# Performance work log

Measured on AMD Instinct MI355X. Metric: run time of the kernel, lower is better.

The kernel has to match this reference:

```python
import jax, jax.numpy as jnp
import numpy as np
from jax import lax

B, T, F, K = 128, 1024, 128, 32


def setup_inputs() -> dict:
    key = jax.random.key(0)
    k1, k2, k3 = jax.random.split(key, 3)
    inp = jax.random.normal(k1, (B, T, F), dtype=jnp.float32)
    mask = jnp.ones((B, T), dtype=bool)
    W_emit = jax.random.normal(k2, (F, K), dtype=jnp.float32) * 0.02
    transition = jax.random.normal(k3, (K, K), dtype=jnp.float32) * 0.1
    return {"input": inp, "mask": mask, "W_emit": W_emit, "transition": transition}


def reference(input, mask, W_emit, transition):
    # emissions: [B, T, K]
    emission = jnp.einsum('btf,fk->btk', input, W_emit)
    alpha0 = emission[:, 0]                      # [B, K]
    em_seq = jnp.swapaxes(emission[:, 1:], 0, 1)  # [T-1, B, K]
    mk_seq = jnp.swapaxes(mask[:, 1:], 0, 1)      # [T-1, B]

    def step(alpha, xs):
        em_t, m_t = xs
        # alpha_t[b,j] = logsumexp_i(alpha[b,i] + transition[i,j]) + em_t[b,j]
        new = jax.scipy.special.logsumexp(alpha[:, :, None] + transition[None], axis=1) + em_t
        alpha = jnp.where(m_t[:, None], new, alpha)
        return alpha, None

    alpha, _ = lax.scan(step, alpha0, (em_seq, mk_seq))
    log_z = jax.scipy.special.logsumexp(alpha, axis=-1)  # [B]
    return jnp.sum(log_z)
```

## Files before the change

### kernel.cpp

```cpp
#include <hip/hip_runtime.h>

#define Bb 128
#define Tt 1024
#define Ff 128
#define Kk 32
#define KS 36
#define KE 36
#define LOG32 3.4657359027997265f

typedef __attribute__((ext_vector_type(8))) short bf16x8;
typedef __attribute__((ext_vector_type(4))) float f32x4;

__device__ __forceinline__ float bf2f(unsigned u) {
    return __uint_as_float(u << 16);
}
__device__ __forceinline__ unsigned short f2bf(float f) {
    unsigned u = __float_as_uint(f);
    u = (u + 0x7fffu + ((u >> 16) & 1u)) >> 16;
    return (unsigned short)u;
}
__device__ __forceinline__ unsigned bfpk(float a, float b) {
    unsigned ua = (__float_as_uint(a) + 0x8000u) >> 16;
    unsigned ub = (__float_as_uint(b) + 0x8000u) & 0xffff0000u;
    return ua | ub;
}

__global__ __launch_bounds__(64, 4) void chunk_kernel(
    const float* __restrict__ inp, const int* __restrict__ mask,
    const float* __restrict__ W, const float* __restrict__ trans,
    unsigned short* __restrict__ SQ)
{
    __shared__ __align__(16) float gl[32 * KE];
    __shared__ __align__(16) unsigned short Sl[32 * KS];
    const int lane = threadIdx.x & 63;
    const int q = lane >> 4, n = lane & 15;
    const int b = blockIdx.x >> 5, c = blockIdx.x & 31;
    const int t0 = c ? c * 32 : 1;
    const int L  = c ? 32 : 31;

    const int* mbp = mask + (long)b * Tt;
    int mybit = (lane < L) ? (mbp[t0 + lane] != 0) : 0;
    const unsigned mbits = (unsigned)__ballot(mybit);

    bf16x8 A0, A1;
    #pragma unroll
    for (int j = 0; j < 8; ++j) {
        A0[j] = (short)f2bf(__expf(trans[(q * 8 + j) * Kk + n]));
        A1[j] = (short)f2bf(__expf(trans[(q * 8 + j) * Kk + 16 + n]));
    }

    const f32x4 zz = {0.f, 0.f, 0.f, 0.f};
    f32x4 E00 = zz, E01 = zz, E10 = zz, E11 = zz;
    const float* xrow = inp + ((long)b * Tt + t0) * Ff;
    #pragma unroll
    for (int kt = 0; kt < 4; ++kt) {
        const int f0 = kt * 32 + q * 8;
        float4 al0 = *(const float4*)&xrow[ n        * Ff + f0];
        float4 al1 = *(const float4*)&xrow[ n        * Ff + f0 + 4];
        float4 ah0 = *(const float4*)&xrow[(n + 16)  * Ff + f0];
        float4 ah1 = *(const float4*)&xrow[(n + 16)  * Ff + f0 + 4];
        uint4 ua = make_uint4(bfpk(al0.x, al0.y), bfpk(al0.z, al0.w),
                              bfpk(al1.x, al1.y), bfpk(al1.z, al1.w));
        uint4 ub = make_uint4(bfpk(ah0.x, ah0.y), bfpk(ah0.z, ah0.w),
                              bfpk(ah1.x, ah1.y), bfpk(ah1.z, ah1.w));
        bf16x8 Alo = __builtin_bit_cast(bf16x8, ua);
        bf16x8 Ahi = __builtin_bit_cast(bf16x8, ub);
        float wl[8], wh[8];
        #pragma unroll
        for (int jj = 0; jj < 8; ++jj) {
            wl[jj] = W[(f0 + jj) * Kk + n];
            wh[jj] = W[(f0 + jj) * Kk + 16 + n];
        }
        uint4 uc = make_uint4(bfpk(wl[0], wl[1]), bfpk(wl[2], wl[3]),
                              bfpk(wl[4], wl[5]), bfpk(wl[6], wl[7]));
        uint4 ud = make_uint4(bfpk(wh[0], wh[1]), bfpk(wh[2], wh[3]),
                              bfpk(wh[4], wh[5]), bfpk(wh[6], wh[7]));
        bf16x8 Blo = __builtin_bit_cast(bf16x8, uc);
        bf16x8 Bhi = __builtin_bit_cast(bf16x8, ud);
        E00 = __builtin_amdgcn_mfma_f32_16x16x32_bf16(Alo, Blo, E00, 0, 0, 0);
        E01 = __builtin_amdgcn_mfma_f32_16x16x32_bf16(Alo, Bhi, E01, 0, 0, 0);
        E10 = __builtin_amdgcn_mfma_f32_16x16x32_bf16(Ahi, Blo, E10, 0, 0, 0);
        E11 = __builtin_amdgcn_mfma_f32_16x16x32_bf16(Ahi, Bhi, E11, 0, 0, 0);
    }
    #pragma unroll
    for (int r = 0; r < 4; ++r) {
        gl[( q * 4 + r)      * KE + n]      = __expf(E00[r] - LOG32);
        gl[( q * 4 + r)      * KE + 16 + n] = __expf(E01[r] - LOG32);
        gl[(16 + q * 4 + r)  * KE + n]      = __expf(E10[r] - LOG32);
        gl[(16 + q * 4 + r)  * KE + 16 + n] = __expf(E11[r] - LOG32);
    }

    for (int i = lane; i < (32 * KS) / 2; i += 64)
        ((unsigned*)Sl)[i] = 0u;
    if (lane < 32) Sl[lane * KS + lane] = 0x3f80;

    for (int s = 0; s < L; ++s) {
        if (!((mbits >> s) & 1u)) continue;
        uint2 xa = *(const uint2*)&Sl[ n       * KS + q * 8];
        uint2 xb = *(const uint2*)&Sl[ n       * KS + q * 8 + 4];
        uint2 ya = *(const uint2*)&Sl[(n + 16) * KS + q * 8];
        uint2 yb = *(const uint2*)&Sl[(n + 16) * KS + q * 8 + 4];
        uint4 u0 = make_uint4(xa.x, xa.y, xb.x, xb.y);
        uint4 u1 = make_uint4(ya.x, ya.y, yb.x, yb.y);
        bf16x8 B0 = __builtin_bit_cast(bf16x8, u0);
        bf16x8 B1 = __builtin_bit_cast(bf16x8, u1);
        f32x4 D00 = __builtin_amdgcn_mfma_f32_16x16x32_bf16(A0, B0, zz, 0, 0, 0);
        f32x4 D01 = __builtin_amdgcn_mfma_f32_16x16x32_bf16(A0, B1, zz, 0, 0, 0);
        f32x4 D10 = __builtin_amdgcn_mfma_f32_16x16x32_bf16(A1, B0, zz, 0, 0, 0);
        f32x4 D11 = __builtin_amdgcn_mfma_f32_16x16x32_bf16(A1, B1, zz, 0, 0, 0);
        float4 g0 = *(const float4*)&gl[s * KE + q * 4];
        float4 g1 = *(const float4*)&gl[s * KE + 16 + q * 4];
        *(uint2*)&Sl[ n       * KS      + q * 4] =
            make_uint2(bfpk(D00[0] * g0.x, D00[1] * g0.y), bfpk(D00[2] * g0.z, D00[3] * g0.w));
        *(uint2*)&Sl[(n + 16) * KS      + q * 4] =
            make_uint2(bfpk(D01[0] * g0.x, D01[1] * g0.y), bfpk(D01[2] * g0.z, D01[3] * g0.w));
        *(uint2*)&Sl[ n       * KS + 16 + q * 4] =
            make_uint2(bfpk(D10[0] * g1.x, D10[1] * g1.y), bfpk(D10[2] * g1.z, D10[3] * g1.w));
        *(uint2*)&Sl[(n + 16) * KS + 16 + q * 4] =
            make_uint2(bfpk(D11[0] * g1.x, D11[1] * g1.y), bfpk(D11[2] * g1.z, D11[3] * g1.w));
    }

    unsigned short* sq = SQ + (long)(b * 32 + c) * 1024;
    #pragma unroll
    for (int it = 0; it < 2; ++it) {
        int f = it * 512 + lane * 8;
        int kk = f >> 5, n0 = f & 31;
        unsigned v[4];
        #pragma unroll
        for (int e = 0; e < 4; ++e) {
            unsigned lo = Sl[(n0 + 2 * e    ) * KS + kk];
            unsigned hi = Sl[(n0 + 2 * e + 1) * KS + kk];
            v[e] = lo | (hi << 16);
        }
        *(uint4*)(sq + f) = make_uint4(v[0], v[1], v[2], v[3]);
    }
}

__global__ __launch_bounds__(64) void apply_kernel(
    const float* __restrict__ inp, const int* __restrict__ mask,
    const float* __restrict__ W, const unsigned short* __restrict__ SQ,
    float* __restrict__ out)
{
    const int b = blockIdx.x, lane = threadIdx.x & 63, k = lane & 31;
    const int* mbp = mask + (long)b * Tt;

    const unsigned short* sqb = SQ + (long)b * 32 * 1024;
    uint4 cur[4], nxt[4];
    #pragma unroll
    for (int e = 0; e < 4; ++e) cur[e] = *(const uint4*)(sqb + k * 32 + 8 * e);
    #pragma unroll
    for (int e = 0; e < 4; ++e) nxt[e] = *(const uint4*)(sqb + 1024 + k * 32 + 8 * e);

    int cnt = 0;
    #pragma unroll
    for (int it = 0; it < 16; ++it) cnt += (mbp[it * 64 + lane] != 0) ? 1 : 0;
    #pragma unroll
    for (int off = 32; off; off >>= 1) cnt += __shfl_xor(cnt, off);
    cnt -= (mbp[0] != 0) ? 1 : 0;

    const float* x0 = inp + (long)b * Tt * Ff;
    float a0 = 0.f;
    #pragma unroll 4
    for (int f = 0; f < Ff; ++f)
        a0 = fmaf(x0[f], W[f * Kk + k], a0);

    float c0 = __int_as_float(__builtin_amdgcn_readlane(__float_as_int(a0), 0));
    float p = __expf(a0 - c0);
    float csum = c0 + (float)cnt * LOG32;

    for (int c = 0; c < 32; ++c) {
        uint4 pf[4];
        if (c + 2 < 32) {
            const unsigned short* s2 = sqb + (c + 2) * 1024 + k * 32;
            #pragma unroll
            for (int e = 0; e < 4; ++e) pf[e] = *(const uint4*)(s2 + 8 * e);
        }
        const int pi = __float_as_int(p);
        float q0 = 0.f, q1 = 0.f, q2 = 0.f, q3 = 0.f;
        #define RL(j) __int_as_float(__builtin_amdgcn_readlane(pi, (j)))
        #define ACC2(word, j, acc) \
            acc = fmaf(bf2f((word) & 0xffffu), RL(j), acc); \
            acc = fmaf(bf2f((word) >> 16),     RL((j) + 1), acc);
        ACC2(cur[0].x,  0, q0) ACC2(cur[0].y,  2, q0) ACC2(cur[0].z,  4, q0) ACC2(cur[0].w,  6, q0)
        ACC2(cur[1].x,  8, q1) ACC2(cur[1].y, 10, q1) ACC2(cur[1].z, 12, q1) ACC2(cur[1].w, 14, q1)
        ACC2(cur[2].x, 16, q2) ACC2(cur[2].y, 18, q2) ACC2(cur[2].z, 20, q2) ACC2(cur[2].w, 22, q2)
        ACC2(cur[3].x, 24, q3) ACC2(cur[3].y, 26, q3) ACC2(cur[3].z, 28, q3) ACC2(cur[3].w, 30, q3)
        #undef ACC2
        #undef RL
        float qq = (q0 + q1) + (q2 + q3);
        if (c == 15) {
            float s0 = __int_as_float(__builtin_amdgcn_readlane(__float_as_int(qq), 0));
            csum += __logf(s0);
            qq *= (1.0f / s0);
        }
        p = qq;
        #pragma unroll
        for (int e = 0; e < 4; ++e) { cur[e] = nxt[e]; nxt[e] = pf[e]; }
    }

    float sum = p;
    #pragma unroll
    for (int off = 16; off > 0; off >>= 1)
        sum += __shfl_xor(sum, off);
    if (lane == 0)
        atomicAdd(out, csum + __logf(sum));
}

extern "C" void kernel_launch(void* const* d_in, const int* in_sizes, int n_in,
                              void* d_out, int out_size, void* d_ws, size_t ws_size,
                              hipStream_t stream)
{
    const float* inp   = (const float*)d_in[0];
    const int*   mask  = (const int*)d_in[1];
    const float* W     = (const float*)d_in[2];
    const float* trans = (const float*)d_in[3];
    float* out = (float*)d_out;
    unsigned short* SQ = (unsigned short*)d_ws;

    hipMemsetAsync(d_out, 0, sizeof(float), stream);
    chunk_kernel<<<dim3(Bb * 32), dim3(64), 0, stream>>>(inp, mask, W, trans, SQ);
    apply_kernel<<<dim3(Bb), dim3(64), 0, stream>>>(inp, mask, W, SQ, out);
}
```

Before: 132.0 us.

## Fuse chunk and apply kernels via last-block-done atomic counter per batch

Merges the two kernels into one. The last of the 32 chunk blocks for each batch row, found with an atomic counter and thread fences, runs the sequential apply phase. This removes a kernel launch and the grid-wide dependency gap, at the cost of an extra memset for the counters and tail blocks that run serially. It also widens the shared-memory row stride so B fragments load as single 16-byte reads, and uses the hip bf16 pair conversion intrinsic (round-to-nearest-even) instead of manual packing.

```diff
diff --git a/kernel.cpp b/kernel.cpp
--- a/kernel.cpp
+++ b/kernel.cpp
@@ -1,10 +1,11 @@
 #include <hip/hip_runtime.h>
+#include <hip/hip_bf16.h>
 
 #define Bb 128
 #define Tt 1024
 #define Ff 128
 #define Kk 32
-#define KS 36
+#define KS 40
 #define KE 36
 #define LOG32 3.4657359027997265f
 
@@ -19,16 +20,18 @@
     u = (u + 0x7fffu + ((u >> 16) & 1u)) >> 16;
     return (unsigned short)u;
 }
-__device__ __forceinline__ unsigned bfpk(float a, float b) {
-    unsigned ua = (__float_as_uint(a) + 0x8000u) >> 16;
-    unsigned ub = (__float_as_uint(b) + 0x8000u) & 0xffff0000u;
-    return ua | ub;
-}
-
-__global__ __launch_bounds__(64, 4) void chunk_kernel(
+__device__ __forceinline__ unsigned bfpk2(float a, float b) {
+    __hip_bfloat162 h = __float22bfloat162_rn(make_float2(a, b));
+    unsigned u;
+    __builtin_memcpy(&u, &h, sizeof(u));
+    return u;
+}
+
+__global__ __launch_bounds__(64, 4) void crf_kernel(
     const float* __restrict__ inp, const int* __restrict__ mask,
     const float* __restrict__ W, const float* __restrict__ trans,
-    unsigned short* __restrict__ SQ)
+    unsigned short* __restrict__ SQ, int* __restrict__ cnt,
+    float* __restrict__ out)
 {
     __shared__ __align__(16) float gl[32 * KE];
     __shared__ __align__(16) unsigned short Sl[32 * KS];
@@ -59,24 +62,26 @@
         float4 al1 = *(const float4*)&xrow[ n        * Ff + f0 + 4];
         float4 ah0 = *(const float4*)&xrow[(n + 16)  * Ff + f0];
         float4 ah1 = *(const float4*)&xrow[(n + 16)  * Ff + f0 + 4];
-        uint4 ua = make_uint4(bfpk(al0.x, al0.y), bfpk(al0.z, al0.w),
-                              bfpk(al1.x, al1.y), bfpk(al1.z, al1.w));
-        uint4 ub = make_uint4(bfpk(ah0.x, ah0.y), bfpk(ah0.z, ah0.w),
-                              bfpk(ah1.x, ah1.y), bfpk(ah1.z, ah1.w));
-        bf16x8 Alo = __builtin_bit_cast(bf16x8, ua);
-        bf16x8 Ahi = __builtin_bit_cast(bf16x8, ub);
+        uint4 ua = make_uint4(bfpk2(al0.x, al0.y), bfpk2(al0.z, al0.w),
+                              bfpk2(al1.x, al1.y), bfpk2(al1.z, al1.w));
+        uint4 ub = make_uint4(bfpk2(ah0.x, ah0.y), bfpk2(ah0.z, ah0.w),
+                              bfpk2(ah1.x, ah1.y), bfpk2(ah1.z, ah1.w));
+        bf16x8 Alo, Ahi;
+        __builtin_memcpy(&Alo, &ua, 16);
+        __builtin_memcpy(&Ahi, &ub, 16);
         float wl[8], wh[8];
         #pragma unroll
         for (int jj = 0; jj < 8; ++jj) {
             wl[jj] = W[(f0 + jj) * Kk + n];
             wh[jj] = W[(f0 + jj) * Kk + 16 + n];
         }
-        uint4 uc = make_uint4(bfpk(wl[0], wl[1]), bfpk(wl[2], wl[3]),
-                              bfpk(wl[4], wl[5]), bfpk(wl[6], wl[7]));
-        uint4 ud = make_uint4(bfpk(wh[0], wh[1]), bfpk(wh[2], wh[3]),
-                              bfpk(wh[4], wh[5]), bfpk(wh[6], wh[7]));
-        bf16x8 Blo = __builtin_bit_cast(bf16x8, uc);
-        bf16x8 Bhi = __builtin_bit_cast(bf16x8, ud);
+        uint4 uc = make_uint4(bfpk2(wl[0], wl[1]), bfpk2(wl[2], wl[3]),
+                              bfpk2(wl[4], wl[5]), bfpk2(wl[6], wl[7]));
+        uint4 ud = make_uint4(bfpk2(wh[0], wh[1]), bfpk2(wh[2], wh[3]),
+                              bfpk2(wh[4], wh[5]), bfpk2(wh[6], wh[7]));
+        bf16x8 Blo, Bhi;
+        __builtin_memcpy(&Blo, &uc, 16);
+        __builtin_memcpy(&Bhi, &ud, 16);
         E00 = __builtin_amdgcn_mfma_f32_16x16x32_bf16(Alo, Blo, E00, 0, 0, 0);
         E01 = __builtin_amdgcn_mfma_f32_16x16x32_bf16(Alo, Bhi, E01, 0, 0, 0);
         E10 = __builtin_amdgcn_mfma_f32_16x16x32_bf16(Ahi, Blo, E10, 0, 0, 0);
@@ -96,14 +101,11 @@
 
     for (int s = 0; s < L; ++s) {
         if (!((mbits >> s) & 1u)) continue;
-        uint2 xa = *(const uint2*)&Sl[ n       * KS + q * 8];
-        uint2 xb = *(const uint2*)&Sl[ n       * KS + q * 8 + 4];
-        uint2 ya = *(const uint2*)&Sl[(n + 16) * KS + q * 8];
-        uint2 yb = *(const uint2*)&Sl[(n + 16) * KS + q * 8 + 4];
-        uint4 u0 = make_uint4(xa.x, xa.y, xb.x, xb.y);
-        uint4 u1 = make_uint4(ya.x, ya.y, yb.x, yb.y);
-        bf16x8 B0 = __builtin_bit_cast(bf16x8, u0);
-        bf16x8 B1 = __builtin_bit_cast(bf16x8, u1);
+        uint4 u0 = *(const uint4*)&Sl[ n       * KS + q * 8];
+        uint4 u1 = *(const uint4*)&Sl[(n + 16) * KS + q * 8];
+        bf16x8 B0, B1;
+        __builtin_memcpy(&B0, &u0, 16);
+        __builtin_memcpy(&B1, &u1, 16);
         f32x4 D00 = __builtin_amdgcn_mfma_f32_16x16x32_bf16(A0, B0, zz, 0, 0, 0);
         f32x4 D01 = __builtin_amdgcn_mfma_f32_16x16x32_bf16(A0, B1, zz, 0, 0, 0);
         f32x4 D10 = __builtin_amdgcn_mfma_f32_16x16x32_bf16(A1, B0, zz, 0, 0, 0);
@@ -111,13 +113,13 @@
         float4 g0 = *(const float4*)&gl[s * KE + q * 4];
         float4 g1 = *(const float4*)&gl[s * KE + 16 + q * 4];
         *(uint2*)&Sl[ n       * KS      + q * 4] =
-            make_uint2(bfpk(D00[0] * g0.x, D00[1] * g0.y), bfpk(D00[2] * g0.z, D00[3] * g0.w));
+            make_uint2(bfpk2(D00[0] * g0.x, D00[1] * g0.y), bfpk2(D00[2] * g0.z, D00[3] * g0.w));
         *(uint2*)&Sl[(n + 16) * KS      + q * 4] =
-            make_uint2(bfpk(D01[0] * g0.x, D01[1] * g0.y), bfpk(D01[2] * g0.z, D01[3] * g0.w));
+            make_uint2(bfpk2(D01[0] * g0.x, D01[1] * g0.y), bfpk2(D01[2] * g0.z, D01[3] * g0.w));
         *(uint2*)&Sl[ n       * KS + 16 + q * 4] =
-            make_uint2(bfpk(D10[0] * g1.x, D10[1] * g1.y), bfpk(D10[2] * g1.z, D10[3] * g1.w));
+            make_uint2(bfpk2(D10[0] * g1.x, D10[1] * g1.y), bfpk2(D10[2] * g1.z, D10[3] * g1.w));
         *(uint2*)&Sl[(n + 16) * KS + 16 + q * 4] =
-            make_uint2(bfpk(D11[0] * g1.x, D11[1] * g1.y), bfpk(D11[2] * g1.z, D11[3] * g1.w));
+            make_uint2(bfpk2(D11[0] * g1.x, D11[1] * g1.y), bfpk2(D11[2] * g1.z, D11[3] * g1.w));
     }
 
     unsigned short* sq = SQ + (long)(b * 32 + c) * 1024;
@@ -134,16 +136,15 @@
         }
         *(uint4*)(sq + f) = make_uint4(v[0], v[1], v[2], v[3]);
     }
-}
-
-__global__ __launch_bounds__(64) void apply_kernel(
-    const float* __restrict__ inp, const int* __restrict__ mask,
-    const float* __restrict__ W, const unsigned short* __restrict__ SQ,
-    float* __restrict__ out)
-{
-    const int b = blockIdx.x, lane = threadIdx.x & 63, k = lane & 31;
-    const int* mbp = mask + (long)b * Tt;
-
+
+    __threadfence();
+    int old = 0;
+    if (lane == 0) old = atomicAdd(&cnt[b], 1);
+    old = __shfl(old, 0);
+    if (old != 31) return;
+    __threadfence();
+
+    const int k = lane & 31;
     const unsigned short* sqb = SQ + (long)b * 32 * 1024;
     uint4 cur[4], nxt[4];
     #pragma unroll
@@ -151,12 +152,12 @@
     #pragma unroll
     for (int e = 0; e < 4; ++e) nxt[e] = *(const uint4*)(sqb + 1024 + k * 32 + 8 * e);
 
-    int cnt = 0;
-    #pragma unroll
-    for (int it = 0; it < 16; ++it) cnt += (mbp[it * 64 + lane] != 0) ? 1 : 0;
-    #pragma unroll
-    for (int off = 32; off; off >>= 1) cnt += __shfl_xor(cnt, off);
-    cnt -= (mbp[0] != 0) ? 1 : 0;
+    int cc = 0;
+    #pragma unroll
+    for (int it = 0; it < 16; ++it) cc += (mbp[it * 64 + lane] != 0) ? 1 : 0;
+    #pragma unroll
+    for (int off = 32; off; off >>= 1) cc += __shfl_xor(cc, off);
+    cc -= (mbp[0] != 0) ? 1 : 0;
 
     const float* x0 = inp + (long)b * Tt * Ff;
     float a0 = 0.f;
@@ -166,12 +167,12 @@
 
     float c0 = __int_as_float(__builtin_amdgcn_readlane(__float_as_int(a0), 0));
     float p = __expf(a0 - c0);
-    float csum = c0 + (float)cnt * LOG32;
-
-    for (int c = 0; c < 32; ++c) {
+    float csum = c0 + (float)cc * LOG32;
+
+    for (int ci = 0; ci < 32; ++ci) {
         uint4 pf[4];
-        if (c + 2 < 32) {
-            const unsigned short* s2 = sqb + (c + 2) * 1024 + k * 32;
+        if (ci + 2 < 32) {
+            const unsigned short* s2 = sqb + (ci + 2) * 1024 + k * 32;
             #pragma unroll
             for (int e = 0; e < 4; ++e) pf[e] = *(const uint4*)(s2 + 8 * e);
         }
@@ -188,7 +189,7 @@
         #undef ACC2
         #undef RL
         float qq = (q0 + q1) + (q2 + q3);
-        if (c == 15) {
+        if (ci == 15) {
             float s0 = __int_as_float(__builtin_amdgcn_readlane(__float_as_int(qq), 0));
             csum += __logf(s0);
             qq *= (1.0f / s0);
@@ -215,9 +216,11 @@
     const float* W     = (const float*)d_in[2];
     const float* trans = (const float*)d_in[3];
     float* out = (float*)d_out;
+    const size_t sq_bytes = (size_t)Bb * 32 * 1024 * 2;
     unsigned short* SQ = (unsigned short*)d_ws;
-
-    hipMemsetAsync(d_out, 0, sizeof(float), stream);
-    chunk_kernel<<<dim3(Bb * 32), dim3(64), 0, stream>>>(inp, mask, W, trans, SQ);
-    apply_kernel<<<dim3(Bb), dim3(64), 0, stream>>>(inp, mask, W, SQ, out);
-}
+    int* cnt = (int*)((char*)d_ws + sq_bytes);
+
+    (void)hipMemsetAsync(d_out, 0, sizeof(float), stream);
+    (void)hipMemsetAsync(cnt, 0, Bb * sizeof(int), stream);
+    crf_kernel<<<dim3(Bb * 32), dim3(64), 0, stream>>>(inp, mask, W, trans, SQ, cnt, out);
+}
```

New measurement: 235.8 us. 78.6% more time.
